# Performance work log

Hardware: AMD Instinct MI355X
Metric: run time of the kernel (lower is better)

## Reference

```python
import jax, jax.numpy as jnp
import numpy as np

NEG = -1e9  # large negative instead of -inf for numerical safety; masked rows are zeroed afterwards
LN_EPS = 1e-5


def layer_norm(x, g, b):
    mu = jnp.mean(x, axis=-1, keepdims=True)
    var = jnp.mean(jnp.square(x - mu), axis=-1, keepdims=True)
    return (x - mu) * jax.lax.rsqrt(var + LN_EPS) * g + b


def causal_conv1d(x_bct, w_oik):
    # x: [B, C, T], w: [O, I, K]; left-pad by K-1 (causal ConvNorm)
    k = w_oik.shape[-1]
    return jax.lax.conv_general_dilated(
        x_bct, w_oik, window_strides=(1,), padding=[(k - 1, 0)],
        dimension_numbers=('NCH', 'OIH', 'NCH'))


def setup_inputs() -> dict:
    key = jax.random.key(0)
    ks = jax.random.split(key, 8)
    B, T, D, H, F, K = 2, 2048, 1024, 16, 4096, 3
    MAXLEN = 4096
    x = jax.random.normal(ks[0], (B, T, D), dtype=jnp.float32)
    lengths = jnp.array([2048, 1536])
    x_mask = jnp.arange(T)[None, :] >= lengths[:, None]  # True = padded
    std = 0.02
    pos_table = jax.random.normal(ks[1], (MAXLEN, D), dtype=jnp.float32) * std
    w_qkv = jax.random.normal(ks[2], (3 * D, D), dtype=jnp.float32) * std
    w_o = jax.random.normal(ks[3], (D, D), dtype=jnp.float32) * std
    conv1_w = jax.random.normal(ks[4], (F, D, K), dtype=jnp.float32) * std
    conv2_w = jax.random.normal(ks[5], (D, F, K), dtype=jnp.float32) * std
    return {
        'x': x, 'x_mask': x_mask, 'pos_table': pos_table,
        'w_qkv': w_qkv, 'w_o': w_o,
        'ln1_g': jnp.ones((D,)), 'ln1_b': jnp.zeros((D,)),
        'ln2_g': jnp.ones((D,)), 'ln2_b': jnp.zeros((D,)),
        'conv1_w': conv1_w, 'conv2_w': conv2_w,
    }


def reference(x, x_mask, pos_table, w_qkv, w_o, ln1_g, ln1_b, ln2_g, ln2_b, conv1_w, conv2_w):
    B, T, D = x.shape
    H = 16
    dh = D // H
    scale = dh ** -0.5

    # ---- self-attention block (pre-norm) ----
    q_in = layer_norm(x, ln1_g, ln1_b)
    q_in = q_in + pos_table[:T][None]  # learnable positional embeddings
    qkv = jnp.einsum('btd,ed->bte', q_in, w_qkv).reshape(B, T, 3, H, dh)
    q, k, v = qkv[:, :, 0], qkv[:, :, 1], qkv[:, :, 2]
    scores = jnp.einsum('bthd,bshd->bhts', q, k) * scale  # [B,H,T,T]
    pad_mask = x_mask[:, None, :, None]                    # mask padded query rows
    causal = jnp.tril(jnp.ones((T, T), dtype=bool))[None, None]
    scores = jnp.where(pad_mask | ~causal, NEG, scores)
    prob = jax.nn.softmax(scores, axis=-1)
    prob = jnp.where(pad_mask, 0.0, prob)
    y = jnp.einsum('bhts,bshd->bthd', prob, v).reshape(B, T, D)
    y = jnp.einsum('btd,ed->bte', y, w_o)
    x = x + y  # dropout p=0

    # ---- positionwise causal conv FFN (pre-norm) ----
    h = layer_norm(x, ln2_g, ln2_b)
    h = jnp.transpose(h, (0, 2, 1))           # [B, D, T]
    h = causal_conv1d(h, conv1_w)             # [B, F, T]
    h = jax.nn.gelu(h, approximate=True)
    h = causal_conv1d(h, conv2_w)             # [B, D, T]
    h = jnp.transpose(h, (0, 2, 1))
    x = x + h
    return x
```

## Files before the change

### kernel.cpp

```cpp
#include <hip/hip_runtime.h>
#include <stdint.h>
#include <math.h>

#define T_SEQ 2048
#define D_MODEL 1024
#define NHEAD 16
#define DH 64
#define F_FF 4096
#define TP (T_SEQ + 2)

typedef unsigned short u16;
typedef float f32x4 __attribute__((ext_vector_type(4)));
typedef __bf16 bf16x8 __attribute__((ext_vector_type(8)));

__device__ __forceinline__ u16 f2bf(float f){
  unsigned u = __float_as_uint(f);
  u = u + 0x7fffu + ((u >> 16) & 1u);
  return (u16)(u >> 16);
}
__device__ __forceinline__ float b2f(u16 h){ return __uint_as_float(((unsigned)h) << 16); }

__device__ __forceinline__ float gelu_f(float x){
  const float c = 0.7978845608028654f;
  float u = c * (x + 0.044715f * x * x * x);
  float e = __expf(-2.0f * u);
  return x * __builtin_amdgcn_rcpf(1.0f + e);
}

#define AS1 __attribute__((address_space(1)))
#define AS3 __attribute__((address_space(3)))
__device__ __forceinline__ void async_cp16(void* lds, const void* g){
  __builtin_amdgcn_global_load_lds((AS1 void*)(void*)g, (AS3 void*)lds, 16, 0, 0);
}

__device__ __forceinline__ float fload(const void* p, size_t i, unsigned isbf){
  return isbf ? b2f(((const u16*)p)[i]) : ((const float*)p)[i];
}

__global__ void detect_dtype(const u16* __restrict__ x, unsigned* __restrict__ flags){
  unsigned e = ((unsigned)x[threadIdx.x] >> 7) & 0xFF;
  bool good = (e == 0 || (e >= 90 && e <= 150));
  unsigned long long b = __ballot(good);
  if (threadIdx.x == 0) flags[0] = (b == ~0ULL) ? 1u : 0u;
}

__global__ __launch_bounds__(256) void canon_mask(const unsigned char* __restrict__ raw,
                                                  unsigned char* __restrict__ canon){
  int i = blockIdx.x * 256 + threadIdx.x;
  if (i >= 2 * T_SEQ) return;
  unsigned char v;
  if (raw[3584]) {
    v = raw[i] != 0;
  } else if (raw[7168]) {
    v = ((const u16*)raw)[i] != 0;
  } else if (raw[14336]) {
    v = ((const int*)raw)[i] != 0;
  } else {
    v = ((const long long*)raw)[i] != 0;
  }
  canon[i] = v;
}

__global__ __launch_bounds__(256)
void cast_any2bf(const void* __restrict__ in, u16* __restrict__ out, int n,
                 const unsigned* __restrict__ flags){
  int i = (blockIdx.x * 256 + threadIdx.x) * 4;
  if (i >= n) return;
  if (flags[0]){
    *(ushort4*)(out + i) = *(const ushort4*)((const u16*)in + i);
  } else {
    float4 v = *(const float4*)((const float*)in + i);
    ushort4 o = { f2bf(v.x), f2bf(v.y), f2bf(v.z), f2bf(v.w) };
    *(ushort4*)(out + i) = o;
  }
}

__global__ __launch_bounds__(256)
void cast_out(const float* __restrict__ in, const float* __restrict__ res,
              void* __restrict__ out, int n, const unsigned* __restrict__ flags){
  int i = (blockIdx.x * 256 + threadIdx.x) * 4;
  if (i >= n) return;
  float4 v = *(const float4*)(in + i);
  float4 r = *(const float4*)(res + i);
  v.x += r.x; v.y += r.y; v.z += r.z; v.w += r.w;
  if (flags[0]){
    ushort4 o = { f2bf(v.x), f2bf(v.y), f2bf(v.z), f2bf(v.w) };
    *(ushort4*)((u16*)out + i) = o;
  } else {
    *(float4*)((float*)out + i) = v;
  }
}

template<int INX1>
__global__ __launch_bounds__(256)
void ln_kernel(const void* __restrict__ inv, const void* __restrict__ g,
               const void* __restrict__ be, const void* __restrict__ pos,
               u16* __restrict__ out, int addpos, int padout,
               const unsigned* __restrict__ flags)
{
  const unsigned isbf = flags[0];
  const int r = blockIdx.x;
  const int bb = r >> 11, tt = r & (T_SEQ - 1);
  const size_t ib = (size_t)r * D_MODEL + threadIdx.x * 4;
  float v0, v1, v2, v3;
  if (INX1){
    float4 v = *(const float4*)((const float*)inv + ib);
    v0 = v.x; v1 = v.y; v2 = v.z; v3 = v.w;
  } else if (isbf){
    ushort4 u = *(const ushort4*)((const u16*)inv + ib);
    v0 = b2f(u.x); v1 = b2f(u.y); v2 = b2f(u.z); v3 = b2f(u.w);
  } else {
    float4 v = *(const float4*)((const float*)inv + ib);
    v0 = v.x; v1 = v.y; v2 = v.z; v3 = v.w;
  }
  float s  = v0 + v1 + v2 + v3;
  float s2 = v0*v0 + v1*v1 + v2*v2 + v3*v3;
  #pragma unroll
  for (int o = 1; o < 64; o <<= 1){ s += __shfl_xor(s, o); s2 += __shfl_xor(s2, o); }
  __shared__ float w1[4], w2[4];
  int w = threadIdx.x >> 6;
  if ((threadIdx.x & 63) == 0){ w1[w] = s; w2[w] = s2; }
  __syncthreads();
  float S  = w1[0] + w1[1] + w1[2] + w1[3];
  float S2 = w2[0] + w2[1] + w2[2] + w2[3];
  float mu  = S * (1.f / 1024.f);
  float var = S2 * (1.f / 1024.f) - mu * mu;
  float rs  = rsqrtf(var + 1e-5f);
  int d0 = threadIdx.x * 4;
  float o0 = (v0 - mu) * rs * fload(g, d0 + 0, isbf) + fload(be, d0 + 0, isbf);
  float o1 = (v1 - mu) * rs * fload(g, d0 + 1, isbf) + fload(be, d0 + 1, isbf);
  float o2 = (v2 - mu) * rs * fload(g, d0 + 2, isbf) + fload(be, d0 + 2, isbf);
  float o3 = (v3 - mu) * rs * fload(g, d0 + 3, isbf) + fload(be, d0 + 3, isbf);
  if (addpos){
    size_t pb = (size_t)tt * D_MODEL + d0;
    o0 += fload(pos, pb + 0, isbf);
    o1 += fload(pos, pb + 1, isbf);
    o2 += fload(pos, pb + 2, isbf);
    o3 += fload(pos, pb + 3, isbf);
  }
  size_t orow = padout ? ((size_t)bb * TP + tt + 2) * (size_t)D_MODEL
                       : (size_t)r * D_MODEL;
  ushort4 ov = { f2bf(o0), f2bf(o1), f2bf(o2), f2bf(o3) };
  *(ushort4*)(out + orow + d0) = ov;
}

__global__ __launch_bounds__(256)
void conv_w_split(const void* __restrict__ in, u16* __restrict__ out, int lg2C,
                  const unsigned* __restrict__ flags){
  int i = blockIdx.x * 256 + threadIdx.x;
  if (i >= 4096 * 1024) return;
  const unsigned isbf = flags[0];
  const int C = 1 << lg2C;
  int c = i & (C - 1);
  size_t sb = (size_t)i * 3;
  size_t ob = (size_t)(i >> lg2C) * 3 * C + c;
  out[ob]         = f2bf(fload(in, sb + 0, isbf));
  out[ob + C]     = f2bf(fload(in, sb + 1, isbf));
  out[ob + 2 * C] = f2bf(fload(in, sb + 2, isbf));
}

__global__ __launch_bounds__(256)
void zero_pads(u16* __restrict__ h2pad, u16* __restrict__ g1pad){
  int tid = blockIdx.x * 256 + threadIdx.x;
  if (tid < 2 * 2 * D_MODEL){
    int b = tid >> 11; int off = tid & (2 * D_MODEL - 1);
    h2pad[(size_t)b * TP * D_MODEL + off] = 0;
  }
  if (tid < 2 * 2 * F_FF){
    int b = tid >> 13; int off = tid & (2 * F_FF - 1);
    g1pad[(size_t)b * TP * F_FF + off] = 0;
  }
}

template<int MODE>
__global__ __launch_bounds__(256)
void gemm_bt(const u16* __restrict__ A, const u16* __restrict__ B,
             const void* __restrict__ res, void* __restrict__ outp,
             int N, int Kin, int lg2Kin, int nseg, long Abstride,
             const unsigned* __restrict__ flags)
{
  __shared__ u16 smA[128 * 32];
  __shared__ u16 smB[128 * 32];
  const int tid = threadIdx.x;
  const int m0 = blockIdx.y * 128;
  const int n0 = blockIdx.x * 128;
  const int Ktot = Kin * nseg;
  const int segz = (MODE == 4) ? blockIdx.z : 0;

  long abase[2]; const u16* bbase[2];
  #pragma unroll
  for (int i = 0; i < 2; ++i){
    int r = m0 + i * 64 + (tid >> 2);
    int bb = r >> 11, tt = r & (T_SEQ - 1);
    abase[i] = (long)bb * Abstride + (long)tt * Kin + (tid & 3) * 8;
    bbase[i] = B + (long)(n0 + i * 64 + (tid >> 2)) * Ktot + (tid & 3) * 8;
  }

  f32x4 acc[4][4];
  #pragma unroll
  for (int i = 0; i < 4; ++i)
    #pragma unroll
    for (int j = 0; j < 4; ++j){ f32x4 z = {0.f,0.f,0.f,0.f}; acc[i][j] = z; }

  const int wm = (tid >> 6) & 1, wn = (tid >> 7) & 1;
  const int lane = tid & 63, lq = lane >> 4, lr = lane & 15;
  const int aoff = (wm * 64 + lr) * 32 + lq * 8;
  const int boff = (wn * 64 + lr) * 32 + lq * 8;

  const int Kloop = (MODE == 4) ? Kin : Ktot;
  for (int k0 = 0; k0 < Kloop; k0 += 32){
    long aso, bso;
    if (MODE == 4){
      aso = (long)segz * Kin + k0;
      bso = aso;
    } else {
      int seg = k0 >> lg2Kin;
      int j0  = k0 & (Kin - 1);
      aso = (long)seg * Kin + j0;
      bso = k0;
    }
    #pragma unroll
    for (int i = 0; i < 2; ++i){
      async_cp16(&smA[i * 2048 + tid * 8], A + abase[i] + aso);
      async_cp16(&smB[i * 2048 + tid * 8], bbase[i] + bso);
    }
    __syncthreads();
    bf16x8 af[4], bfv[4];
    #pragma unroll
    for (int mi = 0; mi < 4; ++mi) af[mi]  = *(const bf16x8*)&smA[aoff + mi * 512];
    #pragma unroll
    for (int ni = 0; ni < 4; ++ni) bfv[ni] = *(const bf16x8*)&smB[boff + ni * 512];
    #pragma unroll
    for (int mi = 0; mi < 4; ++mi)
      #pragma unroll
      for (int ni = 0; ni < 4; ++ni)
        acc[mi][ni] = __builtin_amdgcn_mfma_f32_16x16x32_bf16(af[mi], bfv[ni], acc[mi][ni], 0, 0, 0);
    __syncthreads();
  }

  const unsigned isbf = (MODE == 1 || MODE == 3) ? flags[0] : 0;
  #pragma unroll
  for (int mi = 0; mi < 4; ++mi){
    #pragma unroll
    for (int ni = 0; ni < 4; ++ni){
      int row0 = m0 + wm * 64 + mi * 16 + lq * 4;
      int col  = n0 + wn * 64 + ni * 16 + lr;
      if (MODE == 0){
        ushort4 pv = { f2bf(acc[mi][ni][0]), f2bf(acc[mi][ni][1]),
                       f2bf(acc[mi][ni][2]), f2bf(acc[mi][ni][3]) };
        if (col < 2 * D_MODEL){
          #pragma unroll
          for (int rr = 0; rr < 4; ++rr)
            ((u16*)outp)[(size_t)(row0 + rr) * N + col] = ((const u16*)&pv)[rr];
        } else {
          int hh = (col - 2 * D_MODEL) >> 6, dd = (col - 2 * D_MODEL) & 63;
          int bb = row0 >> 11, tt = row0 & (T_SEQ - 1);
          *(ushort4*)((u16*)const_cast<void*>(res) +
                      ((size_t)(bb * NHEAD + hh) * 64 + dd) * T_SEQ + tt) = pv;
        }
      } else {
        #pragma unroll
        for (int rr = 0; rr < 4; ++rr){
          int row = row0 + rr;
          float v = acc[mi][ni][rr];
          size_t idx = (size_t)row * N + col;
          if (MODE == 1){
            ((float*)outp)[idx] = v + fload(res, idx, isbf);
          } else if (MODE == 2){
            int bb = row >> 11, tt = row & (T_SEQ - 1);
            ((u16*)outp)[((size_t)bb * TP + tt + 2) * N + col] = f2bf(gelu_f(v));
          } else if (MODE == 3){
            float ov = v + ((const float*)res)[idx];
            if (isbf) ((u16*)outp)[idx] = f2bf(ov);
            else      ((float*)outp)[idx] = ov;
          } else {
            atomicAdd((float*)outp + idx, v);
          }
        }
      }
    }
  }
}

__global__ __launch_bounds__(256)
void attn_mfma(const u16* __restrict__ qkv, const u16* __restrict__ vT,
               const unsigned char* __restrict__ mask, u16* __restrict__ y)
{
  const int qb = blockIdx.x, h = blockIdx.y, b = blockIdx.z;
  const int q0 = qb * 64;
  const int tid = threadIdx.x;

  if (mask[b * T_SEQ + q0]){
    int r = tid >> 2, c4 = (tid & 3) * 16;
    u16* yp = y + (size_t)(b * T_SEQ + q0 + r) * D_MODEL + h * DH + c4;
    ushort4 z = {0, 0, 0, 0};
    #pragma unroll
    for (int c = 0; c < 4; ++c) *(ushort4*)(yp + c * 4) = z;
    return;
  }

  const int w = tid >> 6, lane = tid & 63;
  const int quad = lane >> 4, lr = lane & 15;

  __shared__ u16 Ks[64 * 72];
  __shared__ u16 Vs[64 * 72];
  __shared__ u16 Ps[64 * 72];

  bf16x8 aq0, aq1;
  {
    const u16* qp = qkv + (size_t)(b * T_SEQ + q0 + w * 16 + lr) * 3072 + h * DH + quad * 8;
    aq0 = *(const bf16x8*)qp;
    aq1 = *(const bf16x8*)(qp + 32);
  }

  f32x4 acc_o[4];
  #pragma unroll
  for (int i = 0; i < 4; ++i){ f32x4 z = {0.f,0.f,0.f,0.f}; acc_o[i] = z; }
  float mrow[4] = {-1e30f, -1e30f, -1e30f, -1e30f};
  float lrow[4] = {0.f, 0.f, 0.f, 0.f};

  const int sr = tid >> 3, sg = tid & 7;

  for (int it = 0; it <= qb; ++it){
    const int s0 = it * 64;
    #pragma unroll
    for (int rr = 0; rr < 64; rr += 32){
      int row = sr + rr;
      *(uint4*)&Ks[row * 72 + sg * 8] =
        *(const uint4*)(qkv + (size_t)(b * T_SEQ + s0 + row) * 3072 + D_MODEL + h * DH + sg * 8);
      *(uint4*)&Vs[row * 72 + sg * 8] =
        *(const uint4*)(vT + ((size_t)(b * NHEAD + h) * 64 + row) * T_SEQ + s0 + sg * 8);
    }
    __syncthreads();

    f32x4 accs[4];
    #pragma unroll
    for (int nt = 0; nt < 4; ++nt){
      f32x4 z = {0.f, 0.f, 0.f, 0.f};
      bf16x8 bk0 = *(const bf16x8*)&Ks[(nt * 16 + lr) * 72 + quad * 8];
      bf16x8 bk1 = *(const bf16x8*)&Ks[(nt * 16 + lr) * 72 + quad * 8 + 32];
      z = __builtin_amdgcn_mfma_f32_16x16x32_bf16(aq0, bk0, z, 0, 0, 0);
      z = __builtin_amdgcn_mfma_f32_16x16x32_bf16(aq1, bk1, z, 0, 0, 0);
      accs[nt] = z;
    }

    const bool diag = (it == qb);
    float sv[4][4], mx[4];
    #pragma unroll
    for (int rr = 0; rr < 4; ++rr) mx[rr] = -1e30f;
    #pragma unroll
    for (int nt = 0; nt < 4; ++nt){
      #pragma unroll
      for (int rr = 0; rr < 4; ++rr){
        float s = accs[nt][rr] * 0.125f;
        if (diag && (nt * 16 + lr) > (w * 16 + quad * 4 + rr)) s = -1e30f;
        sv[nt][rr] = s;
        mx[rr] = fmaxf(mx[rr], s);
      }
    }
    #pragma unroll
    for (int o = 1; o < 16; o <<= 1){
      #pragma unroll
      for (int rr = 0; rr < 4; ++rr) mx[rr] = fmaxf(mx[rr], __shfl_xor(mx[rr], o));
    }
    float alpha[4], psum[4];
    #pragma unroll
    for (int rr = 0; rr < 4; ++rr){
      float mnew = fmaxf(mrow[rr], mx[rr]);
      alpha[rr] = __expf(mrow[rr] - mnew);
      mrow[rr] = mnew;
      psum[rr] = 0.f;
    }
    #pragma unroll
    for (int nt = 0; nt < 4; ++nt){
      #pragma unroll
      for (int rr = 0; rr < 4; ++rr){
        float p = __expf(sv[nt][rr] - mrow[rr]);
        psum[rr] += p;
        Ps[(w * 16 + quad * 4 + rr) * 72 + nt * 16 + lr] = f2bf(p);
      }
    }
    #pragma unroll
    for (int o = 1; o < 16; o <<= 1){
      #pragma unroll
      for (int rr = 0; rr < 4; ++rr) psum[rr] += __shfl_xor(psum[rr], o);
    }
    #pragma unroll
    for (int rr = 0; rr < 4; ++rr) lrow[rr] = lrow[rr] * alpha[rr] + psum[rr];
    #pragma unroll
    for (int nt = 0; nt < 4; ++nt)
      #pragma unroll
      for (int rr = 0; rr < 4; ++rr) acc_o[nt][rr] *= alpha[rr];

    bf16x8 ap0 = *(const bf16x8*)&Ps[(w * 16 + lr) * 72 + quad * 8];
    bf16x8 ap1 = *(const bf16x8*)&Ps[(w * 16 + lr) * 72 + quad * 8 + 32];
    #pragma unroll
    for (int nt = 0; nt < 4; ++nt){
      bf16x8 bv0 = *(const bf16x8*)&Vs[(nt * 16 + lr) * 72 + quad * 8];
      bf16x8 bv1 = *(const bf16x8*)&Vs[(nt * 16 + lr) * 72 + quad * 8 + 32];
      acc_o[nt] = __builtin_amdgcn_mfma_f32_16x16x32_bf16(ap0, bv0, acc_o[nt], 0, 0, 0);
      acc_o[nt] = __builtin_amdgcn_mfma_f32_16x16x32_bf16(ap1, bv1, acc_o[nt], 0, 0, 0);
    }
    __syncthreads();
  }

  #pragma unroll
  for (int rr = 0; rr < 4; ++rr){
    int qg = q0 + w * 16 + quad * 4 + rr;
    float inv = 1.0f / lrow[rr];
    bool rm = mask[b * T_SEQ + qg] != 0;
    #pragma unroll
    for (int nt = 0; nt < 4; ++nt){
      float v = rm ? 0.f : acc_o[nt][rr] * inv;
      y[(size_t)(b * T_SEQ + qg) * D_MODEL + h * DH + nt * 16 + lr] = f2bf(v);
    }
  }
}

extern "C" void kernel_launch(void* const* d_in, const int* in_sizes, int n_in,
                              void* d_out, int out_size, void* d_ws, size_t ws_size,
                              hipStream_t stream)
{
  const void* x       = d_in[0];
  const unsigned char* xmask_raw = (const unsigned char*)d_in[1];
  const void* pos     = d_in[2];
  const void* w_qkv   = d_in[3];
  const void* w_o     = d_in[4];
  const void* ln1_g   = d_in[5];
  const void* ln1_b   = d_in[6];
  const void* ln2_g   = d_in[7];
  const void* ln2_b   = d_in[8];
  const void* conv1_w = d_in[9];
  const void* conv2_w = d_in[10];

  char* ws = (char*)d_ws;
  size_t o = 0;
  auto alloc = [&](size_t bytes){ size_t cur = o; o += (bytes + 255) & ~(size_t)255; return cur; };
  unsigned* flags = (unsigned*)(ws + alloc(256));
  unsigned char* maskc = (unsigned char*)(ws + alloc(2 * T_SEQ));
  float* x1   = (float*)(ws + alloc((size_t)2 * T_SEQ * D_MODEL * 4));
  char* h2slab = ws + alloc((size_t)2 * TP * D_MODEL * 2);
  u16* g1pad  = (u16*)(ws + alloc((size_t)2 * TP * F_FF * 2));
  u16* slabA  = (u16*)(ws + alloc((size_t)4096 * 3072 * 2));
  u16* qy     = (u16*)(ws + alloc((size_t)4096 * 1024 * 2));
  char* vslab = ws + alloc((size_t)4096 * 1024 * 4);
  u16* vt     = (u16*)vslab;
  float* xc   = (float*)vslab;

  u16* wqkv_c = (u16*)h2slab;
  u16* wo_c   = (u16*)h2slab + (size_t)3072 * 1024;
  u16* h2pad  = (u16*)h2slab;
  u16* qin    = qy;
  u16* qkvb   = slabA;
  u16* yb     = qy;
  u16* W1cat  = slabA;
  u16* W2cat  = slabA;

  detect_dtype<<<1, 64, 0, stream>>>((const u16*)x, flags);
  canon_mask<<<16, 256, 0, stream>>>(xmask_raw, maskc);
  cast_any2bf<<<3072 * 1024 / 4 / 256, 256, 0, stream>>>(w_qkv, wqkv_c, 3072 * 1024, flags);
  cast_any2bf<<<1024 * 1024 / 4 / 256, 256, 0, stream>>>(w_o, wo_c, 1024 * 1024, flags);
  ln_kernel<0><<<4096, 256, 0, stream>>>(x, ln1_g, ln1_b, pos, qin, 1, 0, flags);
  gemm_bt<0><<<dim3(24, 32), 256, 0, stream>>>(qin, wqkv_c, vt, qkvb,
                                               3072, 1024, 10, 1, (long)T_SEQ * 1024, flags);
  attn_mfma<<<dim3(32, 16, 2), 256, 0, stream>>>(qkvb, vt, maskc, yb);
  gemm_bt<1><<<dim3(8, 32), 256, 0, stream>>>(yb, wo_c, x, x1,
                                              1024, 1024, 10, 1, (long)T_SEQ * 1024, flags);
  hipMemsetAsync(xc, 0, (size_t)4096 * 1024 * 4, stream);
  conv_w_split<<<4096 * 1024 / 256, 256, 0, stream>>>(conv1_w, W1cat, 10, flags);
  zero_pads<<<64, 256, 0, stream>>>(h2pad, g1pad);
  ln_kernel<1><<<4096, 256, 0, stream>>>(x1, ln2_g, ln2_b, nullptr, h2pad, 0, 1, flags);
  gemm_bt<2><<<dim3(32, 32), 256, 0, stream>>>(h2pad, W1cat, nullptr, g1pad,
                                               4096, 1024, 10, 3, (long)TP * 1024, flags);
  conv_w_split<<<4096 * 1024 / 256, 256, 0, stream>>>(conv2_w, W2cat, 12, flags);
  gemm_bt<4><<<dim3(8, 32, 3), 256, 0, stream>>>(g1pad, W2cat, nullptr, xc,
                                                 1024, 4096, 12, 3, (long)TP * 4096, flags);
  cast_out<<<4096 * 1024 / 4 / 256, 256, 0, stream>>>(xc, x1, d_out, 4096 * 1024, flags);
}
```

Before: 747.3 us.

## Add 256x256 tiled 512-thread GEMM with 4-stage async pipeline for conv1

Replaces the conv1 GEMM (gelu epilogue) with a new kernel using 256x256 output tiles, 8 waves, a 4-buffer LDS ring filled by async global-to-LDS copies, and split A/B staging interleaved with MFMA phases using barriers and priority hints. The aim is more operand reuse per block and better overlap of memory loads with matrix math on the largest GEMM. The cost is 128KB of LDS per block and heavy register use for the 8x4 accumulator array, which limits occupancy. The causal taps are handled through the strided A addressing (Kin 1024 versus Ktot 3072), which relies on the padded layout.

Measured after the change: 683.2 us. 1.09x faster.

```diff
diff --git a/kernel.cpp b/kernel.cpp
--- a/kernel.cpp
+++ b/kernel.cpp
@@ -282,6 +282,129 @@
   }
 }
 
+__device__ __forceinline__ void ktile8(
+    f32x4 (&acc)[8][4], u16 (*L)[16384], int buf, int abase, int bbase,
+    const u16* __restrict__ A, const long (&asrc)[2], const u16* const (&bsrc)[2],
+    const int (&adst)[2], const int (&bdst)[2], int kt, bool stage_ok)
+{
+  const u16* Lp = L[buf];
+  bf16x8 bfr[4], a0[4];
+  #pragma unroll
+  for (int nf = 0; nf < 4; ++nf) bfr[nf] = *(const bf16x8*)&Lp[bbase + nf * 512];
+  #pragma unroll
+  for (int j = 0; j < 4; ++j) a0[j] = *(const bf16x8*)&Lp[abase + j * 512];
+  if (stage_ok){
+    u16* Ld = L[(kt + 3) & 3];
+    #pragma unroll
+    for (int s = 0; s < 2; ++s)
+      async_cp16(&Ld[adst[s]], A + asrc[s] + (long)(kt + 3) * 32);
+  }
+  __builtin_amdgcn_s_barrier();
+  __builtin_amdgcn_sched_barrier(0);
+  __builtin_amdgcn_s_setprio(1);
+  #pragma unroll
+  for (int j = 0; j < 4; ++j)
+    #pragma unroll
+    for (int nf = 0; nf < 4; ++nf)
+      acc[j][nf] = __builtin_amdgcn_mfma_f32_16x16x32_bf16(a0[j], bfr[nf], acc[j][nf], 0, 0, 0);
+  __builtin_amdgcn_s_setprio(0);
+  __builtin_amdgcn_s_barrier();
+  __builtin_amdgcn_sched_barrier(0);
+  bf16x8 a1[4];
+  #pragma unroll
+  for (int j = 0; j < 4; ++j) a1[j] = *(const bf16x8*)&Lp[abase + (4 + j) * 512];
+  if (stage_ok){
+    u16* Ld = L[(kt + 3) & 3];
+    #pragma unroll
+    for (int s = 0; s < 2; ++s)
+      async_cp16(&Ld[bdst[s]], bsrc[s] + (long)(kt + 3) * 32);
+  }
+  __builtin_amdgcn_s_barrier();
+  __builtin_amdgcn_sched_barrier(0);
+  __builtin_amdgcn_s_setprio(1);
+  #pragma unroll
+  for (int j = 0; j < 4; ++j)
+    #pragma unroll
+    for (int nf = 0; nf < 4; ++nf)
+      acc[4 + j][nf] = __builtin_amdgcn_mfma_f32_16x16x32_bf16(a1[j], bfr[nf], acc[4 + j][nf], 0, 0, 0);
+  __builtin_amdgcn_s_setprio(0);
+}
+
+template<int MODE>
+__global__ __launch_bounds__(512, 2)
+void gemm8(const u16* __restrict__ A, const u16* __restrict__ Bm,
+           u16* __restrict__ outp, int N, int Kin, int Ktot, long Abstride)
+{
+  __shared__ u16 L[4][16384];
+  const int tid = threadIdx.x;
+  const int m0 = blockIdx.y * 256, n0 = blockIdx.x * 256;
+  const int NKT = Ktot >> 5;
+
+  const int rl = tid >> 2;
+  const int ch = (tid & 3) ^ (rl & 3);
+  long asrc[2]; const u16* bsrc[2]; int adst[2], bdst[2];
+  #pragma unroll
+  for (int s = 0; s < 2; ++s){
+    int r = m0 + s * 128 + rl;
+    int bb = r >> 11, tt = r & (T_SEQ - 1);
+    asrc[s] = (long)bb * Abstride + (long)tt * Kin + ch * 8;
+    bsrc[s] = Bm + (long)(n0 + s * 128 + rl) * Ktot + ch * 8;
+    adst[s] = (s * 512 + tid) * 8;
+    bdst[s] = 8192 + adst[s];
+  }
+
+  const int w = tid >> 6, lane = tid & 63;
+  const int wm = w >> 2, wn = w & 3;
+  const int quad = lane >> 4, lr = lane & 15;
+  const int xq = quad ^ (lr & 3);
+  const int abase = ((wm * 128 + lr) * 4 + xq) * 8;
+  const int bbase = 8192 + ((wn * 64 + lr) * 4 + xq) * 8;
+
+  f32x4 acc[8][4];
+  #pragma unroll
+  for (int i = 0; i < 8; ++i)
+    #pragma unroll
+    for (int j = 0; j < 4; ++j){ f32x4 z = {0.f,0.f,0.f,0.f}; acc[i][j] = z; }
+
+  #pragma unroll
+  for (int j = 0; j < 3; ++j){
+    #pragma unroll
+    for (int s = 0; s < 2; ++s) async_cp16(&L[j][adst[s]], A + asrc[s] + j * 32);
+    #pragma unroll
+    for (int s = 0; s < 2; ++s) async_cp16(&L[j][bdst[s]], bsrc[s] + j * 32);
+  }
+
+  int kt = 0;
+  for (; kt < NKT - 2; ++kt){
+    asm volatile("s_waitcnt vmcnt(8)" ::: "memory");
+    __builtin_amdgcn_s_barrier();
+    __builtin_amdgcn_sched_barrier(0);
+    ktile8(acc, L, kt & 3, abase, bbase, A, asrc, bsrc, adst, bdst, kt, kt + 3 < NKT);
+  }
+  asm volatile("s_waitcnt vmcnt(4)" ::: "memory");
+  __builtin_amdgcn_s_barrier();
+  __builtin_amdgcn_sched_barrier(0);
+  ktile8(acc, L, (NKT - 2) & 3, abase, bbase, A, asrc, bsrc, adst, bdst, NKT - 2, false);
+  asm volatile("s_waitcnt vmcnt(0)" ::: "memory");
+  __builtin_amdgcn_s_barrier();
+  __builtin_amdgcn_sched_barrier(0);
+  ktile8(acc, L, (NKT - 1) & 3, abase, bbase, A, asrc, bsrc, adst, bdst, NKT - 1, false);
+
+  #pragma unroll
+  for (int mf = 0; mf < 8; ++mf){
+    #pragma unroll
+    for (int nf = 0; nf < 4; ++nf){
+      int col = n0 + wn * 64 + nf * 16 + lr;
+      #pragma unroll
+      for (int rr = 0; rr < 4; ++rr){
+        int row = m0 + wm * 128 + mf * 16 + quad * 4 + rr;
+        int bb = row >> 11, tt = row & (T_SEQ - 1);
+        outp[((size_t)(bb * TP + tt + 2)) * N + col] = f2bf(gelu_f(acc[mf][nf][rr]));
+      }
+    }
+  }
+}
+
 __global__ __launch_bounds__(256)
 void attn_mfma(const u16* __restrict__ qkv, const u16* __restrict__ vT,
                const unsigned char* __restrict__ mask, u16* __restrict__ y)
@@ -470,8 +593,8 @@
   conv_w_split<<<4096 * 1024 / 256, 256, 0, stream>>>(conv1_w, W1cat, 10, flags);
   zero_pads<<<64, 256, 0, stream>>>(h2pad, g1pad);
   ln_kernel<1><<<4096, 256, 0, stream>>>(x1, ln2_g, ln2_b, nullptr, h2pad, 0, 1, flags);
-  gemm_bt<2><<<dim3(32, 32), 256, 0, stream>>>(h2pad, W1cat, nullptr, g1pad,
-                                               4096, 1024, 10, 3, (long)TP * 1024, flags);
+  gemm8<2><<<dim3(16, 16), 512, 0, stream>>>(h2pad, W1cat, g1pad,
+                                             4096, 1024, 3072, (long)TP * 1024);
   conv_w_split<<<4096 * 1024 / 256, 256, 0, stream>>>(conv2_w, W2cat, 12, flags);
   gemm_bt<4><<<dim3(8, 32, 3), 256, 0, stream>>>(g1pad, W2cat, nullptr, xc,
                                                  1024, 4096, 12, 3, (long)TP * 4096, flags);
```
